# Performance work log

Hardware: AMD Instinct MI355X
Metric: run time of the kernel (lower is better)

Reference implementation:

```python
import jax, jax.numpy as jnp
import numpy as np

N_NODES = 50000
N_EDGES = 600000
D = 128
L = 3


def setup_inputs() -> dict:
    key = jax.random.key(0)
    ks = jax.random.split(key, 6)
    x = jax.random.normal(ks[0], (N_NODES, D), dtype=jnp.float32)
    edge_index = jax.random.randint(ks[1], (2, N_EDGES), 0, N_NODES, dtype=jnp.int64)
    # Glorot-ish scale for 128x128 linears
    s = 1.0 / np.sqrt(D)
    W_l = jax.random.normal(ks[2], (L, D, D), dtype=jnp.float32) * s
    b_l = jnp.zeros((L, D), dtype=jnp.float32)
    W_r = jax.random.normal(ks[3], (L, D, D), dtype=jnp.float32) * s
    W_out = jax.random.normal(ks[4], (D, 1), dtype=jnp.float32) * s
    b_out = jnp.zeros((1,), dtype=jnp.float32)
    return {"x": x, "edge_index": edge_index, "W_l": W_l, "b_l": b_l,
            "W_r": W_r, "W_out": W_out, "b_out": b_out}


def reference(x, edge_index, W_l, b_l, W_r, W_out, b_out):
    # PyG SAGEConv (aggr='mean', root_weight=True):
    #   out_i = lin_l(mean_{j: (j->i)} x_j) + lin_r(x_i)
    src = edge_index[0]
    dst = edge_index[1]
    n = x.shape[0]
    deg = jax.ops.segment_sum(jnp.ones(src.shape, x.dtype), dst, num_segments=n)
    inv_deg = (1.0 / jnp.maximum(deg, 1.0))[:, None]  # [N,1]
    h = x
    for i in range(W_l.shape[0]):  # fixed small layer count
        agg = jax.ops.segment_sum(h[src], dst, num_segments=n) * inv_deg  # [N,D]
        h = agg @ W_l[i] + b_l[i] + h @ W_r[i]
        h = jax.nn.relu(h)  # dropout is identity at eval (p=0.0)
    return (h @ W_out + b_out)[:, 0]  # squeeze(-1) -> [N]
```

## Files before the change

### kernel.cpp

```cpp
#include <hip/hip_runtime.h>

#define N_NODES 50000
#define N_EDGES 600000
#define D 128
#define NLAYERS 3
#define ELL_W 64

typedef __attribute__((ext_vector_type(8))) short short8;
typedef __attribute__((ext_vector_type(4))) float floatx4;

__device__ __forceinline__ float bf_lo(unsigned u) { return __uint_as_float(u << 16); }
__device__ __forceinline__ float bf_hi(unsigned u) { return __uint_as_float(u & 0xffff0000u); }
__device__ __forceinline__ unsigned short f2bf(float f) {
    unsigned u = __float_as_uint(f);
    return (unsigned short)((u + 0x7fffu + ((u >> 16) & 1u)) >> 16);
}


#define SEC_A (N_NODES * D / 4)
#define SEC_B (SEC_A + NLAYERS * D * 256)
#define SEC_TOT (SEC_B + N_NODES)

__global__ void cvt_init_kernel(const float* __restrict__ x, const float* __restrict__ Wl,
                                const float* __restrict__ Wr,
                                unsigned short* __restrict__ xb,
                                unsigned short* __restrict__ hb1,
                                unsigned short* __restrict__ hb2,
                                unsigned short* __restrict__ WtF,
                                int* __restrict__ cursor) {
    int i = blockIdx.x * blockDim.x + threadIdx.x;
    if (i < SEC_A) {
        float4 v = ((const float4*)x)[i];
        ushort4 o;
        o.x = f2bf(v.x); o.y = f2bf(v.y); o.z = f2bf(v.z); o.w = f2bf(v.w);
        ((ushort4*)xb)[i] = o;
    } else if (i < SEC_B) {
        int t = i - SEC_A;
        int l = t >> 15;
        int r = t & 32767;
        int f = r >> 3;
        int ii = r & 7;
        int jkt = f >> 6;
        int lane = f & 63;
        int j = jkt >> 3;
        int kt = jkt & 7;
        int half = lane & 15;
        int quad = lane >> 4;
        int n = j * 16 + half;
        int k = kt * 32 + quad * 8 + ii;
        float v = (k < D) ? Wl[(size_t)l * D * D + (size_t)k * D + n]
                          : Wr[(size_t)l * D * D + (size_t)(k - D) * D + n];
        WtF[t] = f2bf(v);
    } else if (i < SEC_TOT) {
        int j = i - SEC_B;
        cursor[j] = 0;
        if (j < D) {
            xb[(size_t)N_NODES * D + j] = 0;
            hb1[(size_t)N_NODES * D + j] = 0;
            hb2[(size_t)N_NODES * D + j] = 0;
        }
    }
}


__global__ void fill_kernel(const int* __restrict__ src, const int* __restrict__ dst,
                            int* __restrict__ cursor, unsigned short* __restrict__ ell) {
    int e = blockIdx.x * blockDim.x + threadIdx.x;
    if (e < N_EDGES) {
        int d_ = dst[e];
        int pos = atomicAdd(&cursor[d_], 1);
        if (pos < ELL_W) ell[(size_t)d_ * ELL_W + pos] = (unsigned short)src[e];
    }
}


template <bool LAST>
__global__ __launch_bounds__(256) void fused_layer_kernel(
    const unsigned short* __restrict__ hin,
    const int* __restrict__ degc, const unsigned short* __restrict__ ell,
    const unsigned short* __restrict__ WtF, const float* __restrict__ bias,
    unsigned short* __restrict__ hout,
    const float* __restrict__ Wout, const float* __restrict__ bout,
    float* __restrict__ out) {
    __shared__ union {
        unsigned short a[32 * 256];
        unsigned short c[32][136];
        float red[32][4];
    } sh;

    int m0 = blockIdx.x * 32;
    int tid = threadIdx.x;

    #pragma unroll
    for (int it = 0; it < 2; ++it) {
        int t = it * 256 + tid;
        int rl = t >> 4;
        int c = t & 15;
        int row = min(m0 + rl, N_NODES - 1);
        uint4 v = *((const uint4*)(hin + (size_t)row * D + c * 8));
        int chunk = (16 + c) ^ (rl & 7);
        *((uint4*)&sh.a[rl * 256 + chunk * 8]) = v;
    }

    {
        int grp = tid >> 4;
        int q = tid & 15;
        for (int half_ = 0; half_ < 2; ++half_) {
            int nl = grp + half_ * 16;
            int node = m0 + nl;
            float a[8] = {0.f, 0.f, 0.f, 0.f, 0.f, 0.f, 0.f, 0.f};
            float b[8] = {0.f, 0.f, 0.f, 0.f, 0.f, 0.f, 0.f, 0.f};
            float w = 0.f;
            if (node < N_NODES) {
                int d = min(degc[node], ELL_W);
                int pd = (d + 3) & ~3;
                int base = node * ELL_W;
                for (int e = 0; e < pd; e += 16) {
                    int cnt = min(pd - e, 16);
                    int idx = ell[base + e + q];
                    for (int j = 0; j < cnt; j += 4) {
                        int rem = d - e - j;
                        int s0 = __shfl(idx, j + 0, 16);
                        int s1 = __shfl(idx, j + 1, 16);
                        int s2 = __shfl(idx, j + 2, 16);
                        int s3 = __shfl(idx, j + 3, 16);
                        s1 = (1 < rem) ? s1 : N_NODES;
                        s2 = (2 < rem) ? s2 : N_NODES;
                        s3 = (3 < rem) ? s3 : N_NODES;
                        uint4 v0 = *((const uint4*)(hin + (size_t)s0 * D + q * 8));
                        uint4 v1 = *((const uint4*)(hin + (size_t)s1 * D + q * 8));
                        uint4 v2 = *((const uint4*)(hin + (size_t)s2 * D + q * 8));
                        uint4 v3 = *((const uint4*)(hin + (size_t)s3 * D + q * 8));
                        a[0] += bf_lo(v0.x); a[1] += bf_hi(v0.x);
                        a[2] += bf_lo(v0.y); a[3] += bf_hi(v0.y);
                        a[4] += bf_lo(v0.z); a[5] += bf_hi(v0.z);
                        a[6] += bf_lo(v0.w); a[7] += bf_hi(v0.w);
                        b[0] += bf_lo(v1.x); b[1] += bf_hi(v1.x);
                        b[2] += bf_lo(v1.y); b[3] += bf_hi(v1.y);
                        b[4] += bf_lo(v1.z); b[5] += bf_hi(v1.z);
                        b[6] += bf_lo(v1.w); b[7] += bf_hi(v1.w);
                        a[0] += bf_lo(v2.x); a[1] += bf_hi(v2.x);
                        a[2] += bf_lo(v2.y); a[3] += bf_hi(v2.y);
                        a[4] += bf_lo(v2.z); a[5] += bf_hi(v2.z);
                        a[6] += bf_lo(v2.w); a[7] += bf_hi(v2.w);
                        b[0] += bf_lo(v3.x); b[1] += bf_hi(v3.x);
                        b[2] += bf_lo(v3.y); b[3] += bf_hi(v3.y);
                        b[4] += bf_lo(v3.z); b[5] += bf_hi(v3.z);
                        b[6] += bf_lo(v3.w); b[7] += bf_hi(v3.w);
                    }
                }
                w = 1.0f / (float)max(d, 1);
            }
            uint4 o;
            o.x = (unsigned)f2bf((a[0] + b[0]) * w) | ((unsigned)f2bf((a[1] + b[1]) * w) << 16);
            o.y = (unsigned)f2bf((a[2] + b[2]) * w) | ((unsigned)f2bf((a[3] + b[3]) * w) << 16);
            o.z = (unsigned)f2bf((a[4] + b[4]) * w) | ((unsigned)f2bf((a[5] + b[5]) * w) << 16);
            o.w = (unsigned)f2bf((a[6] + b[6]) * w) | ((unsigned)f2bf((a[7] + b[7]) * w) << 16);
            int chunk = q ^ (nl & 7);
            *((uint4*)&sh.a[nl * 256 + chunk * 8]) = o;
        }
    }
    __syncthreads();

    int wv = tid >> 6;
    int lane = tid & 63;
    int half = lane & 15;
    int quad = lane >> 4;

    floatx4 acc[2][2];
    #pragma unroll
    for (int mt = 0; mt < 2; mt++)
        #pragma unroll
        for (int jj = 0; jj < 2; jj++)
            acc[mt][jj] = (floatx4){0.f, 0.f, 0.f, 0.f};

    const short8* Bf = (const short8*)WtF;
    #pragma unroll
    for (int kt = 0; kt < 8; kt++) {
        int ch = (kt * 4 + quad) ^ (half & 7);
        short8 a0 = *((const short8*)&sh.a[half * 256 + ch * 8]);
        short8 a1 = *((const short8*)&sh.a[(16 + half) * 256 + ch * 8]);
        #pragma unroll
        for (int jj = 0; jj < 2; jj++) {
            int j = wv * 2 + jj;
            short8 b = Bf[(j * 8 + kt) * 64 + lane];
            acc[0][jj] = __builtin_amdgcn_mfma_f32_16x16x32_bf16(a0, b, acc[0][jj], 0, 0, 0);
            acc[1][jj] = __builtin_amdgcn_mfma_f32_16x16x32_bf16(a1, b, acc[1][jj], 0, 0, 0);
        }
    }
    __syncthreads();

    if (!LAST) {
        #pragma unroll
        for (int jj = 0; jj < 2; jj++) {
            int col = (wv * 2 + jj) * 16 + half;
            float bv = bias[col];
            #pragma unroll
            for (int mt = 0; mt < 2; mt++)
                #pragma unroll
                for (int r = 0; r < 4; r++)
                    sh.c[mt * 16 + quad * 4 + r][col] = f2bf(fmaxf(acc[mt][jj][r] + bv, 0.f));
        }
        __syncthreads();
        #pragma unroll
        for (int it = 0; it < 2; ++it) {
            int t = it * 256 + tid;
            int rl = t >> 4;
            int c = t & 15;
            int row = m0 + rl;
            if (row < N_NODES)
                *((uint4*)(hout + (size_t)row * D + c * 8)) = *((const uint4*)&sh.c[rl][c * 8]);
        }
    } else {
        float vout[2][4] = {{0.f, 0.f, 0.f, 0.f}, {0.f, 0.f, 0.f, 0.f}};
        #pragma unroll
        for (int jj = 0; jj < 2; jj++) {
            int col = (wv * 2 + jj) * 16 + half;
            float bv = bias[col];
            float wo = Wout[col];
            #pragma unroll
            for (int mt = 0; mt < 2; mt++)
                #pragma unroll
                for (int r = 0; r < 4; r++)
                    vout[mt][r] += fmaxf(acc[mt][jj][r] + bv, 0.f) * wo;
        }
        #pragma unroll
        for (int off = 1; off < 16; off <<= 1) {
            #pragma unroll
            for (int mt = 0; mt < 2; mt++)
                #pragma unroll
                for (int r = 0; r < 4; r++)
                    vout[mt][r] += __shfl_xor(vout[mt][r], off, 64);
        }
        if (half == 0) {
            #pragma unroll
            for (int mt = 0; mt < 2; mt++)
                #pragma unroll
                for (int r = 0; r < 4; r++)
                    sh.red[mt * 16 + quad * 4 + r][wv] = vout[mt][r];
        }
        __syncthreads();
        if (tid < 32) {
            int row = m0 + tid;
            if (row < N_NODES)
                out[row] = sh.red[tid][0] + sh.red[tid][1] +
                           sh.red[tid][2] + sh.red[tid][3] + bout[0];
        }
    }
}


extern "C" void kernel_launch(void* const* d_in, const int* in_sizes, int n_in,
                              void* d_out, int out_size, void* d_ws, size_t ws_size,
                              hipStream_t stream) {
    const float* x     = (const float*)d_in[0];
    const int*   edge  = (const int*)d_in[1];
    const float* W_l   = (const float*)d_in[2];
    const float* b_l   = (const float*)d_in[3];
    const float* W_r   = (const float*)d_in[4];
    const float* W_out = (const float*)d_in[5];
    const float* b_out = (const float*)d_in[6];
    float* out = (float*)d_out;

    char* ws = (char*)d_ws;
    size_t off = 0;
    auto alloc = [&](size_t bytes) -> void* {
        void* p = ws + off;
        off += (bytes + 255) & ~(size_t)255;
        return p;
    };
    unsigned short* xb  = (unsigned short*)alloc((size_t)(N_NODES + 1) * D * 2);
    unsigned short* hb1 = (unsigned short*)alloc((size_t)(N_NODES + 1) * D * 2);
    unsigned short* hb2 = (unsigned short*)alloc((size_t)(N_NODES + 1) * D * 2);
    unsigned short* WtF = (unsigned short*)alloc((size_t)NLAYERS * D * 256 * 2);
    int* cursor = (int*)alloc((size_t)N_NODES * sizeof(int));
    unsigned short* ell = (unsigned short*)alloc((size_t)N_NODES * ELL_W * sizeof(unsigned short));

    const int* src = edge;
    const int* dst = edge + N_EDGES;

    cvt_init_kernel<<<(SEC_TOT + 255) / 256, 256, 0, stream>>>(
        x, W_l, W_r, xb, hb1, hb2, WtF, cursor);
    fill_kernel<<<(N_EDGES + 255) / 256, 256, 0, stream>>>(src, dst, cursor, ell);

    const int grid = (N_NODES + 31) / 32;

    fused_layer_kernel<false><<<grid, 256, 0, stream>>>(
        xb, cursor, ell, WtF, b_l, hb1, W_out, b_out, out);
    fused_layer_kernel<false><<<grid, 256, 0, stream>>>(
        hb1, cursor, ell, WtF + (size_t)1 * D * 256, b_l + 1 * D, hb2, W_out, b_out, out);
    fused_layer_kernel<true><<<grid, 256, 0, stream>>>(
        hb2, cursor, ell, WtF + (size_t)2 * D * 256, b_l + 2 * D, hb1, W_out, b_out, out);
}
```

Before: 211.2 us.

## Bucket ELL neighbor lists by source-node range for gather locality

Measured after the change: 223.8 us. +5.9%, slower.

```diff
diff --git a/kernel.cpp b/kernel.cpp
--- a/kernel.cpp
+++ b/kernel.cpp
@@ -4,7 +4,9 @@
 #define N_EDGES 600000
 #define D 128
 #define NLAYERS 3
-#define ELL_W 64
+#define NBUCKET 7
+#define BUCKET_W 16
+#define NODE_STRIDE 128
 
 typedef __attribute__((ext_vector_type(8))) short short8;
 typedef __attribute__((ext_vector_type(4))) float floatx4;
@@ -19,7 +21,7 @@
 
 #define SEC_A (N_NODES * D / 4)
 #define SEC_B (SEC_A + NLAYERS * D * 256)
-#define SEC_TOT (SEC_B + N_NODES)
+#define SEC_TOT (SEC_B + N_NODES * 8)
 
 __global__ void cvt_init_kernel(const float* __restrict__ x, const float* __restrict__ Wl,
                                 const float* __restrict__ Wr,
@@ -67,9 +69,12 @@
                             int* __restrict__ cursor, unsigned short* __restrict__ ell) {
     int e = blockIdx.x * blockDim.x + threadIdx.x;
     if (e < N_EDGES) {
+        int s = src[e];
         int d_ = dst[e];
-        int pos = atomicAdd(&cursor[d_], 1);
-        if (pos < ELL_W) ell[(size_t)d_ * ELL_W + pos] = (unsigned short)src[e];
+        int b = s >> 13;
+        int pos = atomicAdd(&cursor[d_ * 8 + b], 1);
+        if (pos < BUCKET_W)
+            ell[(size_t)d_ * NODE_STRIDE + b * BUCKET_W + pos] = (unsigned short)s;
     }
 }
 
@@ -109,21 +114,27 @@
             int nl = grp + half_ * 16;
             int node = m0 + nl;
             float a[8] = {0.f, 0.f, 0.f, 0.f, 0.f, 0.f, 0.f, 0.f};
-            float b[8] = {0.f, 0.f, 0.f, 0.f, 0.f, 0.f, 0.f, 0.f};
+            float b8[8] = {0.f, 0.f, 0.f, 0.f, 0.f, 0.f, 0.f, 0.f};
             float w = 0.f;
             if (node < N_NODES) {
-                int d = min(degc[node], ELL_W);
-                int pd = (d + 3) & ~3;
-                int base = node * ELL_W;
-                for (int e = 0; e < pd; e += 16) {
-                    int cnt = min(pd - e, 16);
-                    int idx = ell[base + e + q];
-                    for (int j = 0; j < cnt; j += 4) {
-                        int rem = d - e - j;
-                        int s0 = __shfl(idx, j + 0, 16);
-                        int s1 = __shfl(idx, j + 1, 16);
-                        int s2 = __shfl(idx, j + 2, 16);
-                        int s3 = __shfl(idx, j + 3, 16);
+                int dq = (q < 8) ? degc[(size_t)node * 8 + q] : 0;
+                const unsigned short* eb = ell + (size_t)node * NODE_STRIDE;
+                int idxv[NBUCKET];
+                #pragma unroll
+                for (int b = 0; b < NBUCKET; b++) idxv[b] = eb[b * BUCKET_W + q];
+
+                int dsum = 0;
+                #pragma unroll
+                for (int b = 0; b < NBUCKET; b++) {
+                    int d_b = min(__shfl(dq, b, 16), BUCKET_W);
+                    dsum += d_b;
+                    int pd = (d_b + 3) & ~3;
+                    for (int j = 0; j < pd; j += 4) {
+                        int rem = d_b - j;
+                        int s0 = __shfl(idxv[b], j + 0, 16);
+                        int s1 = __shfl(idxv[b], j + 1, 16);
+                        int s2 = __shfl(idxv[b], j + 2, 16);
+                        int s3 = __shfl(idxv[b], j + 3, 16);
                         s1 = (1 < rem) ? s1 : N_NODES;
                         s2 = (2 < rem) ? s2 : N_NODES;
                         s3 = (3 < rem) ? s3 : N_NODES;
@@ -135,27 +146,27 @@
                         a[2] += bf_lo(v0.y); a[3] += bf_hi(v0.y);
                         a[4] += bf_lo(v0.z); a[5] += bf_hi(v0.z);
                         a[6] += bf_lo(v0.w); a[7] += bf_hi(v0.w);
-                        b[0] += bf_lo(v1.x); b[1] += bf_hi(v1.x);
-                        b[2] += bf_lo(v1.y); b[3] += bf_hi(v1.y);
-                        b[4] += bf_lo(v1.z); b[5] += bf_hi(v1.z);
-                        b[6] += bf_lo(v1.w); b[7] += bf_hi(v1.w);
+                        b8[0] += bf_lo(v1.x); b8[1] += bf_hi(v1.x);
+                        b8[2] += bf_lo(v1.y); b8[3] += bf_hi(v1.y);
+                        b8[4] += bf_lo(v1.z); b8[5] += bf_hi(v1.z);
+                        b8[6] += bf_lo(v1.w); b8[7] += bf_hi(v1.w);
                         a[0] += bf_lo(v2.x); a[1] += bf_hi(v2.x);
                         a[2] += bf_lo(v2.y); a[3] += bf_hi(v2.y);
                         a[4] += bf_lo(v2.z); a[5] += bf_hi(v2.z);
                         a[6] += bf_lo(v2.w); a[7] += bf_hi(v2.w);
-                        b[0] += bf_lo(v3.x); b[1] += bf_hi(v3.x);
-                        b[2] += bf_lo(v3.y); b[3] += bf_hi(v3.y);
-                        b[4] += bf_lo(v3.z); b[5] += bf_hi(v3.z);
-                        b[6] += bf_lo(v3.w); b[7] += bf_hi(v3.w);
+                        b8[0] += bf_lo(v3.x); b8[1] += bf_hi(v3.x);
+                        b8[2] += bf_lo(v3.y); b8[3] += bf_hi(v3.y);
+                        b8[4] += bf_lo(v3.z); b8[5] += bf_hi(v3.z);
+                        b8[6] += bf_lo(v3.w); b8[7] += bf_hi(v3.w);
                     }
                 }
-                w = 1.0f / (float)max(d, 1);
+                w = 1.0f / (float)max(dsum, 1);
             }
             uint4 o;
-            o.x = (unsigned)f2bf((a[0] + b[0]) * w) | ((unsigned)f2bf((a[1] + b[1]) * w) << 16);
-            o.y = (unsigned)f2bf((a[2] + b[2]) * w) | ((unsigned)f2bf((a[3] + b[3]) * w) << 16);
-            o.z = (unsigned)f2bf((a[4] + b[4]) * w) | ((unsigned)f2bf((a[5] + b[5]) * w) << 16);
-            o.w = (unsigned)f2bf((a[6] + b[6]) * w) | ((unsigned)f2bf((a[7] + b[7]) * w) << 16);
+            o.x = (unsigned)f2bf((a[0] + b8[0]) * w) | ((unsigned)f2bf((a[1] + b8[1]) * w) << 16);
+            o.y = (unsigned)f2bf((a[2] + b8[2]) * w) | ((unsigned)f2bf((a[3] + b8[3]) * w) << 16);
+            o.z = (unsigned)f2bf((a[4] + b8[4]) * w) | ((unsigned)f2bf((a[5] + b8[5]) * w) << 16);
+            o.w = (unsigned)f2bf((a[6] + b8[6]) * w) | ((unsigned)f2bf((a[7] + b8[7]) * w) << 16);
             int chunk = q ^ (nl & 7);
             *((uint4*)&sh.a[nl * 256 + chunk * 8]) = o;
         }
@@ -273,8 +284,8 @@
     unsigned short* hb1 = (unsigned short*)alloc((size_t)(N_NODES + 1) * D * 2);
     unsigned short* hb2 = (unsigned short*)alloc((size_t)(N_NODES + 1) * D * 2);
     unsigned short* WtF = (unsigned short*)alloc((size_t)NLAYERS * D * 256 * 2);
-    int* cursor = (int*)alloc((size_t)N_NODES * sizeof(int));
-    unsigned short* ell = (unsigned short*)alloc((size_t)N_NODES * ELL_W * sizeof(unsigned short));
+    int* cursor = (int*)alloc((size_t)N_NODES * 8 * sizeof(int));
+    unsigned short* ell = (unsigned short*)alloc((size_t)N_NODES * NODE_STRIDE * sizeof(unsigned short));
 
     const int* src = edge;
     const int* dst = edge + N_EDGES;
```
